# Kernel tuning notes

Measured on AMD Instinct MI355X. Metric: run time of the kernel, lower is better.

The kernel has to match this reference:

```python
import jax, jax.numpy as jnp
import numpy as np

B, C, H, W = 16, 384, 64, 64
S, R, GR = 16, 8, 64
EPS = 1e-6


def setup_inputs() -> dict:
    key = jax.random.key(0)
    ks = jax.random.split(key, 16)
    def rn(k, shape, s):
        return jax.random.normal(k, shape, dtype=jnp.float32) * s
    inp = {"x": jax.random.normal(ks[0], (B, C, H, W), dtype=jnp.float32)}
    i = 1
    for p in ("row", "col"):
        inp[p + "_a_logit"] = jnp.zeros((S,), jnp.float32)
        inp[p + "_U"] = rn(ks[i], (S, R), 0.02); i += 1
        inp[p + "_V"] = rn(ks[i], (S, R), 0.02); i += 1
        inp[p + "_Win"] = rn(ks[i], (S, C), 1.0 / np.sqrt(C)); i += 1
        inp[p + "_bin"] = jnp.zeros((S,), jnp.float32)
        inp[p + "_Wg"] = rn(ks[i], (S, C), 1.0 / np.sqrt(C)); i += 1
        inp[p + "_bg"] = jnp.zeros((S,), jnp.float32)
        inp[p + "_Wout"] = rn(ks[i], (C, S), 1.0 / np.sqrt(S)); i += 1
        inp[p + "_bout"] = jnp.zeros((C,), jnp.float32)
        inp[p + "_Wskip"] = rn(ks[i], (C, C), 1.0 / np.sqrt(C)); i += 1
        inp[p + "_bskip"] = jnp.zeros((C,), jnp.float32)
    inp["g1_w"] = rn(ks[i], (GR, C), 1.0 / np.sqrt(C)); i += 1
    inp["g1_b"] = jnp.zeros((GR,), jnp.float32)
    inp["g2_w"] = rn(ks[i], (C, GR), 1.0 / np.sqrt(GR)); i += 1
    inp["g2_b"] = jnp.zeros((C,), jnp.float32)
    inp["norm_w"] = jnp.ones((C,), jnp.float32)
    inp["norm_b"] = jnpp = jnp.zeros((C,), jnp.float32)
    inp["norm_b"] = jnp.zeros((C,), jnp.float32)
    return inp


def _ssm1d(x, a_logit, U, V, Win, bin_, Wg, bg, Wout, bout, Wskip, bskip, reverse):
    # x: [N, L, D]
    if reverse:
        x = x[:, ::-1]
    u = jnp.einsum('nld,sd->nls', x, Win) + bin_          # [N,L,S]
    g = jax.nn.sigmoid(jnp.einsum('nld,sd->nls', x, Wg) + bg)
    a = jax.nn.sigmoid(a_logit)                            # [S]
    # h_t = a*h + g_t*u_t + h @ (U V^T)^T  ==  h @ (diag(a) + (U V^T)^T) + g_t*u_t
    A = jnp.diag(a) + (U @ V.T).T                          # [S,S]
    gu = jnp.swapaxes(g * u, 0, 1)                         # [L,N,S]
    h0 = jnp.zeros((x.shape[0], a.shape[0]), x.dtype)

    def step(h, gu_t):
        h = h @ A + gu_t
        return h, h

    _, hs = jax.lax.scan(step, h0, gu)                     # [L,N,S]
    hs = jnp.swapaxes(hs, 0, 1)                            # [N,L,S]
    y = (jnp.einsum('nls,ds->nld', hs, Wout) + bout
         + jnp.einsum('nld,ed->nle', x, Wskip) + bskip)
    if reverse:
        y = y[:, ::-1]
    return y


def _forward(x, rp, cp, g1_w, g1_b, g2_w, g2_b, norm_w, norm_b):
    Bx, Cx, Hx, Wx = x.shape
    rows = jnp.transpose(x, (0, 2, 3, 1)).reshape(Bx * Hx, Wx, Cx)
    cols = jnp.transpose(x, (0, 3, 2, 1)).reshape(Bx * Wx, Hx, Cx)
    yr = _ssm1d(rows, *rp, False) + _ssm1d(rows, *rp, True)
    yc = _ssm1d(cols, *cp, False) + _ssm1d(cols, *cp, True)
    yr = jnp.transpose(yr.reshape(Bx, Hx, Wx, Cx), (0, 3, 1, 2))
    yc = jnp.transpose(yc.reshape(Bx, Wx, Hx, Cx), (0, 3, 2, 1))
    y = (yr + yc) * 0.25
    # LayerNorm over channel dim of BCHW
    mean = x.mean(axis=1, keepdims=True)
    var = ((x - mean) ** 2).mean(axis=1, keepdims=True)
    xn = (x - mean) / jnp.sqrt(var + EPS)
    xn = xn * norm_w[None, :, None, None] + norm_b[None, :, None, None]
    # gate: 1x1 conv -> GELU(exact) -> 1x1 conv -> sigmoid
    h1 = jax.nn.gelu(jnp.einsum('bchw,oc->bohw', xn, g1_w) + g1_b[None, :, None, None], approximate=False)
    g = jax.nn.sigmoid(jnp.einsum('bghw,cg->bchw', h1, g2_w) + g2_b[None, :, None, None])
    return g * y + (1.0 - g) * x


def reference(x, row_a_logit, row_U, row_V, row_Win, row_bin, row_Wg, row_bg, row_Wout, row_bout, row_Wskip, row_bskip, col_a_logit, col_U, col_V, col_Win, col_bin, col_Wg, col_bg, col_Wout, col_bout, col_Wskip, col_bskip, g1_w, g1_b, g2_w, g2_b, norm_w, norm_b):
    rp = (row_a_logit, row_U, row_V, row_Win, row_bin, row_Wg, row_bg, row_Wout, row_bout, row_Wskip, row_bskip)
    cp = (col_a_logit, col_U, col_V, col_Win, col_bin, col_Wg, col_bg, col_Wout, col_bout, col_Wskip, col_bskip)
    return _forward(x, rp, cp, g1_w, g1_b, g2_w, g2_b, norm_w, norm_b)
```

## Files before the change

kernel.cpp:

```cpp
#include <hip/hip_runtime.h>
#include <hip/hip_bf16.h>
#include <math.h>

#define PP 4096
#define CCH 384
#define NB 16

using short8 = __attribute__((ext_vector_type(8))) short;
using f32x4  = __attribute__((ext_vector_type(4))) float;

__device__ __forceinline__ float sigmoidf_(float v){ return 1.f/(1.f+expf(-v)); }
__device__ __forceinline__ unsigned int f2bf(float f){
  __hip_bfloat16 h = __float2bfloat16(f);
  return (unsigned int)*reinterpret_cast<unsigned short*>(&h);
}
__device__ __forceinline__ float bf2f(unsigned short u){
  unsigned int w = ((unsigned int)u) << 16;
  return __uint_as_float(w);
}
__device__ __forceinline__ void gload_lds16(const void* g, void* l){
  __builtin_amdgcn_global_load_lds(
      (const __attribute__((address_space(1))) unsigned int*)g,
      (__attribute__((address_space(3))) unsigned int*)l, 16, 0, 0);
}

__global__ __launch_bounds__(256) void k_prep(
    const float* __restrict__ rAl, const float* __restrict__ rU, const float* __restrict__ rV,
    const float* __restrict__ cAl, const float* __restrict__ cU, const float* __restrict__ cV,
    const float* __restrict__ rWs, const float* __restrict__ cWs,
    const float* __restrict__ WinR, const float* __restrict__ WgR,
    const float* __restrict__ WinC, const float* __restrict__ WgC,
    const float* __restrict__ g1w, const float* __restrict__ nw, const float* __restrict__ nb,
    const float* __restrict__ g2w,
    const float* __restrict__ WoR, const float* __restrict__ WoC,
    float* __restrict__ Arow, float* __restrict__ Acol,
    unsigned short* __restrict__ WsumBf, unsigned short* __restrict__ WcatBf,
    unsigned short* __restrict__ g2wBf, unsigned short* __restrict__ WocatBf,
    float* __restrict__ t1, float* __restrict__ t2)
{
  int bid = blockIdx.x, tid = threadIdx.x;
  if (bid < 576) {
    int idx = bid*256 + tid;
    WsumBf[idx] = (unsigned short)f2bf(rWs[idx] + cWs[idx]);
  } else if (bid < 768) {
    int idx = (bid-576)*256 + tid;
    int row = idx / CCH, col = idx - row*CCH;
    float v;
    if      (row < 16)  v = WinR[row*CCH + col];
    else if (row < 32)  v = WgR [(row-16)*CCH + col];
    else if (row < 48)  v = WinC[(row-32)*CCH + col];
    else if (row < 64)  v = WgC [(row-48)*CCH + col];
    else                v = g1w[(row-64)*CCH + col]*nw[col];
    WcatBf[idx] = (unsigned short)f2bf(v);
  } else if (bid < 864) {
    int idx = (bid-768)*256 + tid;
    g2wBf[idx] = (unsigned short)f2bf(g2w[idx]);
  } else if (bid < 912) {
    int idx = (bid-864)*256 + tid;
    int c = idx >> 5, k = idx & 31;
    float v = (k < 16) ? WoR[c*16 + k] : WoC[c*16 + (k-16)];
    WocatBf[idx] = (unsigned short)f2bf(v);
  } else {
    {
      int i = tid >> 4, j = tid & 15;
      float sr = 0.f, sc = 0.f;
      #pragma unroll
      for (int r=0;r<8;++r){ sr += rV[i*8+r]*rU[j*8+r]; sc += cV[i*8+r]*cU[j*8+r]; }
      if (i==j){ sr += sigmoidf_(rAl[i]); sc += sigmoidf_(cAl[i]); }
      Arow[tid] = sr; Acol[tid] = sc;
    }
    if (tid < 64) {
      float s1=0.f, s2=0.f;
      for (int c=0;c<CCH;++c){ s1 += g1w[tid*CCH+c]*nw[c]; s2 += nb[c]*g1w[tid*CCH+c]; }
      t1[tid]=s1; t2[tid]=s2;
    }
  }
}

__global__ __launch_bounds__(256) void k_xf(
    const float* __restrict__ x, const unsigned short* __restrict__ WcatBf,
    const float* __restrict__ binR, const float* __restrict__ bgR,
    const float* __restrict__ binC, const float* __restrict__ bgC,
    const float* __restrict__ t1, const float* __restrict__ t2,
    const float* __restrict__ g1b,
    unsigned short* __restrict__ xbf,
    float* __restrict__ ugr, float* __restrict__ ugc,
    unsigned short* __restrict__ h1bf)
{
  int b = blockIdx.x >> 6, pt = blockIdx.x & 63;
  int t = threadIdx.x;
  int w = t >> 6, l = t & 63;
  int lr = l & 15, kq = l >> 4, kb8 = kq*8;
  int pl = t & 63, g4 = w;

  __shared__ unsigned short xtb[64*64];
  __shared__ float red[512];
  __shared__ float meanS[64], invS[64];

  const float* xb = x + (size_t)b*CCH*PP + pt*64;
  f32x4 acc[2][4] = {};
  float sx = 0.f, sx2 = 0.f;

  float xv[16];
  #pragma unroll
  for (int j=0;j<16;++j) xv[j] = xb[(size_t)(g4*16 + j)*PP + pl];

  const unsigned short* wrow0 = WcatBf + (size_t)(w*32 + lr)*CCH + kb8;
  const unsigned short* wrow1 = wrow0 + 16*CCH;
  unsigned short* xgo = xbf + ((size_t)(b*PP + pt*64))*CCH;

  #pragma unroll
  for (int cc=0; cc<6; ++cc) {
    unsigned int pk[8];
    #pragma unroll
    for (int j=0;j<16;++j){ sx += xv[j]; sx2 += xv[j]*xv[j]; }
    #pragma unroll
    for (int j=0;j<8;++j) pk[j] = f2bf(xv[2*j]) | (f2bf(xv[2*j+1])<<16);
    __syncthreads();
    {
      int kg0 = g4*2, kg1 = g4*2+1;
      uint4 v0 = make_uint4(pk[0],pk[1],pk[2],pk[3]);
      uint4 v1 = make_uint4(pk[4],pk[5],pk[6],pk[7]);
      *(uint4*)&xtb[(size_t)(pl*8 + (kg0 ^ (pl&7)))*8] = v0;
      *(uint4*)&xtb[(size_t)(pl*8 + (kg1 ^ (pl&7)))*8] = v1;
    }
    if (cc < 5) {
      #pragma unroll
      for (int j=0;j<16;++j) xv[j] = xb[(size_t)((cc+1)*64 + g4*16 + j)*PP + pl];
    }
    short8 a0k0 = *(const short8*)(wrow0 + cc*64);
    short8 a0k1 = *(const short8*)(wrow0 + cc*64 + 32);
    short8 a1k0 = *(const short8*)(wrow1 + cc*64);
    short8 a1k1 = *(const short8*)(wrow1 + cc*64 + 32);
    __syncthreads();
    #pragma unroll
    for (int ks=0; ks<2; ++ks){
      int kg = ks*4 + kq;
      #pragma unroll
      for (int nf=0; nf<4; ++nf){
        int pr = nf*16 + lr;
        short8 bv = *(const short8*)&xtb[(size_t)(pr*8 + (kg ^ (pr&7)))*8];
        acc[0][nf] = __builtin_amdgcn_mfma_f32_16x16x32_bf16(ks? a0k1:a0k0, bv, acc[0][nf], 0,0,0);
        acc[1][nf] = __builtin_amdgcn_mfma_f32_16x16x32_bf16(ks? a1k1:a1k0, bv, acc[1][nf], 0,0,0);
      }
    }
    #pragma unroll
    for (int it=0; it<2; ++it){
      int p2 = 32*it + (t>>3), kg2 = t & 7;
      uint4 v = *(const uint4*)&xtb[(size_t)(p2*8 + (kg2 ^ (p2&7)))*8];
      *(uint4*)&xgo[(size_t)p2*CCH + cc*64 + kg2*8] = v;
    }
  }

  __syncthreads();
  red[g4*64 + pl] = sx;
  red[256 + g4*64 + pl] = sx2;
  __syncthreads();
  if (t < 64) {
    float s1 = red[t] + red[64+t] + red[128+t] + red[192+t];
    float s2 = red[256+t] + red[320+t] + red[384+t] + red[448+t];
    float mu = s1 * (1.f/CCH);
    float var = s2 * (1.f/CCH) - mu*mu;
    meanS[t] = mu;
    invS[t]  = rsqrtf(var + 1e-6f);
  }
  __syncthreads();

  if (w < 2) {
    const float* bu = w ? binC : binR;
    const float* bg = w ? bgC  : bgR;
    float* dst = w ? ugc : ugr;
    float bus[4], bgs[4];
    #pragma unroll
    for (int r=0;r<4;++r){ int s = kq*4 + r; bus[r]=bu[s]; bgs[r]=bg[s]; }
    #pragma unroll
    for (int nf=0; nf<4; ++nf){
      size_t pbase = ((size_t)(b*PP + pt*64 + nf*16 + lr))*16;
      #pragma unroll
      for (int r=0;r<4;++r){
        int s = kq*4 + r;
        float u = acc[0][nf][r] + bus[r];
        float g = sigmoidf_(acc[1][nf][r] + bgs[r]);
        dst[pbase + s] = u*g;
      }
    }
  } else {
    int ob = (w-2)*32 + kq*4;
    float t1o[2][4], t2o[2][4], gbo[2][4];
    #pragma unroll
    for (int mi=0;mi<2;++mi)
      #pragma unroll
      for (int r=0;r<4;++r){
        int o = ob + mi*16 + r;
        t1o[mi][r]=t1[o]; t2o[mi][r]=t2[o]; gbo[mi][r]=g1b[o];
      }
    #pragma unroll
    for (int nf=0; nf<4; ++nf){
      int pLoc = nf*16 + lr;
      float mu = meanS[pLoc], iv = invS[pLoc];
      #pragma unroll
      for (int mi=0;mi<2;++mi){
        unsigned int us[4];
        #pragma unroll
        for (int r=0;r<4;++r){
          float pre = iv*(acc[mi][nf][r] - mu*t1o[mi][r]) + t2o[mi][r] + gbo[mi][r];
          float ge = 0.5f*pre*(1.f + erff(pre*0.70710678118654752f));
          us[r] = f2bf(ge);
        }
        uint2 o2; o2.x = us[0] | (us[1]<<16); o2.y = us[2] | (us[3]<<16);
        *reinterpret_cast<uint2*>(h1bf + ((size_t)(b*PP + pt*64 + pLoc))*64 + (w-2)*32 + mi*16 + kq*4) = o2;
      }
    }
  }
}

__global__ __launch_bounds__(64) void k_scan(
    const float* __restrict__ ugr, const float* __restrict__ ugc,
    const float* __restrict__ Arow, const float* __restrict__ Acol,
    unsigned short* __restrict__ hscat)
{
  int g = blockIdx.x*4 + (threadIdx.x >> 4);
  int lane = threadIdx.x & 63;
  int s = lane & 15;
  int base = lane & 48;
  bool isCol = g >= 1024;
  int gg = isCol ? g - 1024 : g;
  int b = gg >> 6, rc = gg & 63;
  const float* ug = isCol ? ugc : ugr;
  const float* A  = isCol ? Acol : Arow;
  int off = isCol ? 16 : 0;
  int p0 = b*PP + (isCol ? rc : rc*64);
  int stride = isCol ? 64 : 1;
  float ac[16];
  #pragma unroll
  for (int i=0;i<16;++i) ac[i] = A[i*16 + s];
  float h[64];
  float hf = 0.f;
  #pragma unroll
  for (int l=0;l<64;++l){
    float gu = ug[((size_t)(p0 + l*stride))*16 + s];
    float t = 0.f;
    #pragma unroll
    for (int i=0;i<16;++i) t += __shfl(hf, base + i, 64) * ac[i];
    hf = t + gu;
    h[l] = hf;
  }
  float hb = 0.f;
  #pragma unroll
  for (int l=63;l>=0;--l){
    float gu = ug[((size_t)(p0 + l*stride))*16 + s];
    float t = 0.f;
    #pragma unroll
    for (int i=0;i<16;++i) t += __shfl(hb, base + i, 64) * ac[i];
    hb = t + gu;
    hscat[((size_t)(p0 + l*stride))*32 + off + s] = (unsigned short)f2bf(h[l] + hb);
  }
}

__global__ __launch_bounds__(512) void k_fused(
    const unsigned short* __restrict__ xbf,
    const unsigned short* __restrict__ WsumBf,
    const unsigned short* __restrict__ h1bf, const unsigned short* __restrict__ g2wBf,
    const unsigned short* __restrict__ hscat, const unsigned short* __restrict__ WocatBf,
    const float* __restrict__ g2b,
    const float* __restrict__ boR, const float* __restrict__ bsR,
    const float* __restrict__ boC, const float* __restrict__ bsC,
    float* __restrict__ outp)
{
  int obid = blockIdx.x;
  int bid = ((obid & 7) * 384) + (obid >> 3);
  int pt = bid & 63; int ct = (bid >> 6) % 3; int b = bid / 192;
  int t = threadIdx.x;
  int w = t >> 6, l = t & 63;
  int lr = l & 15, kq = l >> 4, kb8 = kq * 8;
  int c0 = ct*128;
  int crow = w*16 + kq*4;

  __shared__ unsigned short xt[64*48*8];

  short8 gaw[2], gbv[2][4];
  {
    const unsigned short* hbase = h1bf + ((size_t)(b*PP + pt*64 + lr))*64 + kb8;
    const unsigned short* wbg = g2wBf + (size_t)(c0 + w*16 + lr)*64 + kb8;
    #pragma unroll
    for (int ks=0; ks<2; ++ks){
      gaw[ks] = *(const short8*)(wbg + ks*32);
      #pragma unroll
      for (int nf=0; nf<4; ++nf)
        gbv[ks][nf] = *(const short8*)(hbase + (size_t)nf*16*64 + ks*32);
    }
  }

  {
    const unsigned short* xrow0 = xbf + ((size_t)(b*PP + pt*64))*CCH;
    #pragma unroll
    for (int i=0;i<6;++i){
      int G = w*384 + i*64 + l;
      int p = G/48, kgs = G - p*48;
      int kg = (kgs & ~7) | ((kgs & 7) ^ (p & 7));
      gload_lds16(xrow0 + (size_t)p*CCH + kg*8, &xt[(size_t)G*8]);
    }
  }

  f32x4 gac[4] = {};
  #pragma unroll
  for (int ks=0; ks<2; ++ks)
    #pragma unroll
    for (int nf=0; nf<4; ++nf)
      gac[nf] = __builtin_amdgcn_mfma_f32_16x16x32_bf16(gaw[ks], gbv[ks][nf], gac[nf], 0,0,0);

  __syncthreads();

  f32x4 accS[4] = {};
  const unsigned short* wbS = WsumBf + (size_t)(c0 + w*16 + lr)*CCH + kb8;
  #pragma unroll
  for (int c = 0; c < 6; ++c) {
    short8 a0 = *(const short8*)(wbS + c*64);
    short8 a1 = *(const short8*)(wbS + c*64 + 32);
    #pragma unroll
    for (int ks=0; ks<2; ++ks){
      int kgl = ks*4 + kq;
      #pragma unroll
      for (int nf=0; nf<4; ++nf){
        int pr = nf*16 + lr;
        int kgs = c*8 + (kgl ^ (pr & 7));
        short8 bv = *(const short8*)&xt[(size_t)(pr*48 + kgs)*8];
        accS[nf] = __builtin_amdgcn_mfma_f32_16x16x32_bf16(ks? a1:a0, bv, accS[nf], 0,0,0);
      }
    }
  }

  f32x4 yac[4] = {};
  {
    const unsigned short* hb2 = hscat + ((size_t)(b*PP + pt*64 + lr))*32 + kb8;
    const unsigned short* wo0 = WocatBf + (size_t)(c0 + w*16 + lr)*32 + kb8;
    short8 wa0 = *(const short8*)wo0;
    #pragma unroll
    for (int nf=0; nf<4; ++nf){
      short8 hv = *(const short8*)(hb2 + (size_t)nf*16*32);
      yac[nf] = __builtin_amdgcn_mfma_f32_16x16x32_bf16(wa0, hv, yac[nf], 0,0,0);
    }
  }

  uint2 xres[4];
  {
    int kR = c0 + crow;
    int kgR = kR >> 3, eoff = kR & 7;
    #pragma unroll
    for (int nf=0; nf<4; ++nf){
      int p = nf*16 + lr;
      int kgsR = (kgR & ~7) | ((kgR & 7) ^ (p & 7));
      xres[nf] = *(const uint2*)&xt[(size_t)(p*48 + kgsR)*8 + eoff];
    }
  }

  #pragma unroll
  for (int r=0;r<4;++r){
    int c = c0 + crow + r;
    float cbv = 2.f*(boR[c]+bsR[c]+boC[c]+bsC[c]);
    float gbv = g2b[c];
    #pragma unroll
    for (int nf=0;nf<4;++nf){
      unsigned int word = (r < 2) ? xres[nf].x : xres[nf].y;
      unsigned short us = (r & 1) ? (unsigned short)(word >> 16) : (unsigned short)(word & 0xffff);
      float xv = bf2f(us);
      size_t addr = ((size_t)(b*CCH + c))*PP + pt*64 + nf*16 + lr;
      float y = 0.25f*(yac[nf][r] + 2.f*accS[nf][r] + cbv);
      float gt = sigmoidf_(gac[nf][r] + gbv);
      outp[addr] = gt*y + (1.f-gt)*xv;
    }
  }
}

extern "C" void kernel_launch(void* const* d_in, const int* in_sizes, int n_in,
                              void* d_out, int out_size, void* d_ws, size_t ws_size,
                              hipStream_t stream)
{
  const float* x    = (const float*)d_in[0];
  const float* rAl  = (const float*)d_in[1];
  const float* rU   = (const float*)d_in[2];
  const float* rV   = (const float*)d_in[3];
  const float* rWin = (const float*)d_in[4];
  const float* rbin = (const float*)d_in[5];
  const float* rWg  = (const float*)d_in[6];
  const float* rbg  = (const float*)d_in[7];
  const float* rWo  = (const float*)d_in[8];
  const float* rbo  = (const float*)d_in[9];
  const float* rWs  = (const float*)d_in[10];
  const float* rbs  = (const float*)d_in[11];
  const float* cAl  = (const float*)d_in[12];
  const float* cU   = (const float*)d_in[13];
  const float* cV   = (const float*)d_in[14];
  const float* cWin = (const float*)d_in[15];
  const float* cbin = (const float*)d_in[16];
  const float* cWg  = (const float*)d_in[17];
  const float* cbg  = (const float*)d_in[18];
  const float* cWo  = (const float*)d_in[19];
  const float* cbo  = (const float*)d_in[20];
  const float* cWs  = (const float*)d_in[21];
  const float* cbs  = (const float*)d_in[22];
  const float* g1w  = (const float*)d_in[23];
  const float* g1b  = (const float*)d_in[24];
  const float* g2w  = (const float*)d_in[25];
  const float* g2b  = (const float*)d_in[26];
  const float* nw   = (const float*)d_in[27];
  const float* nb   = (const float*)d_in[28];

  float* ws   = (float*)d_ws;
  float* ugr  = ws;
  float* ugc  = ugr + 1048576;
  float* Arow = ugc + 1048576;
  float* Acol = Arow + 256;
  float* t1   = Acol + 256;
  float* t2   = t1 + 64;
  unsigned short* xbf     = (unsigned short*)(t2 + 64);
  unsigned short* h1bf    = xbf + (size_t)25165824;
  unsigned short* hscat   = h1bf + (size_t)4194304;
  unsigned short* WsumBf  = hscat + (size_t)2097152;
  unsigned short* WcatBf  = WsumBf + 147456;
  unsigned short* g2wBf   = WcatBf + 49152;
  unsigned short* WocatBf = g2wBf + 24576;
  float* outp = (float*)d_out;

  k_prep<<<913, 256, 0, stream>>>(rAl,rU,rV,cAl,cU,cV,rWs,cWs,
                                  rWin,rWg,cWin,cWg,g1w,nw,nb,g2w,rWo,cWo,
                                  Arow,Acol,WsumBf,WcatBf,g2wBf,WocatBf,t1,t2);
  k_xf<<<1024, 256, 0, stream>>>(x, WcatBf, rbin, rbg, cbin, cbg,
                                 t1, t2, g1b, xbf, ugr, ugc, h1bf);
  k_scan<<<512, 64, 0, stream>>>(ugr, ugc, Arow, Acol, hscat);
  k_fused<<<3072, 512, 0, stream>>>(xbf, WsumBf, h1bf, g2wBf,
                                    hscat, WocatBf, g2b,
                                    rbo, rbs, cbo, cbs, outp);
}
```

Before: 189.0 us.

## Split bidirectional scan into parallel directions and widen fused kernel channel tile

The scan kernel now runs forward and backward directions as separate parallel tasks, each writing its own slice of a wider hidden-state buffer. This removes the serial two-pass dependency and the 64-entry register array, at the cost of doubling hidden-state traffic. The fused output kernel now covers all 384 channels per pixel tile with 48 channels per wave, so the x tile in LDS and the h1/hs loads are reused across three channel groups instead of being reloaded by three separate blocks. The Wout folding absorbs the combine scaling, and sigmoid uses fast exp2/rcp intrinsics, with gate values packed to fp16 to limit register pressure.

```diff
diff --git a/kernel.cpp b/kernel.cpp
--- a/kernel.cpp
+++ b/kernel.cpp
@@ -8,8 +8,12 @@
 
 using short8 = __attribute__((ext_vector_type(8))) short;
 using f32x4  = __attribute__((ext_vector_type(4))) float;
+using half2t = __attribute__((ext_vector_type(2))) __fp16;
 
 __device__ __forceinline__ float sigmoidf_(float v){ return 1.f/(1.f+expf(-v)); }
+__device__ __forceinline__ float fast_sig(float v){
+  return __builtin_amdgcn_rcpf(1.f + __builtin_amdgcn_exp2f(-v*1.44269504088896f));
+}
 __device__ __forceinline__ unsigned int f2bf(float f){
   __hip_bfloat16 h = __float2bfloat16(f);
   return (unsigned int)*reinterpret_cast<unsigned short*>(&h);
@@ -55,10 +59,11 @@
   } else if (bid < 864) {
     int idx = (bid-768)*256 + tid;
     g2wBf[idx] = (unsigned short)f2bf(g2w[idx]);
-  } else if (bid < 912) {
+  } else if (bid < 960) {
     int idx = (bid-864)*256 + tid;
-    int c = idx >> 5, k = idx & 31;
-    float v = (k < 16) ? WoR[c*16 + k] : WoC[c*16 + (k-16)];
+    int c = idx >> 6, k = idx & 63;
+    int sel = (k >> 4) & 1;
+    float v = 0.5f * (sel ? WoC[c*16 + (k&15)] : WoR[c*16 + (k&15)]);
     WocatBf[idx] = (unsigned short)f2bf(v);
   } else {
     {
@@ -180,7 +185,7 @@
       for (int r=0;r<4;++r){
         int s = kq*4 + r;
         float u = acc[0][nf][r] + bus[r];
-        float g = sigmoidf_(acc[1][nf][r] + bgs[r]);
+        float g = fast_sig(acc[1][nf][r] + bgs[r]);
         dst[pbase + s] = u*g;
       }
     }
@@ -214,80 +219,74 @@
   }
 }
 
-__global__ __launch_bounds__(64) void k_scan(
+__global__ __launch_bounds__(256) void k_scan(
     const float* __restrict__ ugr, const float* __restrict__ ugc,
     const float* __restrict__ Arow, const float* __restrict__ Acol,
-    unsigned short* __restrict__ hscat)
+    unsigned short* __restrict__ hs2)
 {
-  int g = blockIdx.x*4 + (threadIdx.x >> 4);
+  int W = blockIdx.x*4 + (threadIdx.x >> 6);
   int lane = threadIdx.x & 63;
-  int s = lane & 15;
-  int base = lane & 48;
-  bool isCol = g >= 1024;
-  int gg = isCol ? g - 1024 : g;
+  int tsk = W*4 + (lane >> 4);
+  int s = lane & 15, base = lane & 48;
+  int dir = tsk >> 11;
+  int rem = tsk & 2047;
+  int isCol = rem >> 10;
+  int gg = rem & 1023;
   int b = gg >> 6, rc = gg & 63;
   const float* ug = isCol ? ugc : ugr;
   const float* A  = isCol ? Acol : Arow;
-  int off = isCol ? 16 : 0;
+  int off = dir*32 + isCol*16;
   int p0 = b*PP + (isCol ? rc : rc*64);
   int stride = isCol ? 64 : 1;
   float ac[16];
   #pragma unroll
   for (int i=0;i<16;++i) ac[i] = A[i*16 + s];
-  float h[64];
-  float hf = 0.f;
-  #pragma unroll
-  for (int l=0;l<64;++l){
-    float gu = ug[((size_t)(p0 + l*stride))*16 + s];
-    float t = 0.f;
-    #pragma unroll
-    for (int i=0;i<16;++i) t += __shfl(hf, base + i, 64) * ac[i];
-    hf = t + gu;
-    h[l] = hf;
-  }
-  float hb = 0.f;
-  #pragma unroll
-  for (int l=63;l>=0;--l){
-    float gu = ug[((size_t)(p0 + l*stride))*16 + s];
-    float t = 0.f;
-    #pragma unroll
-    for (int i=0;i<16;++i) t += __shfl(hb, base + i, 64) * ac[i];
-    hb = t + gu;
-    hscat[((size_t)(p0 + l*stride))*32 + off + s] = (unsigned short)f2bf(h[l] + hb);
-  }
-}
-
-__global__ __launch_bounds__(512) void k_fused(
+  float h = 0.f;
+  #pragma unroll 4
+  for (int st=0; st<64; ++st){
+    int l2 = dir ? (63-st) : st;
+    float gu = ug[((size_t)(p0 + l2*stride))*16 + s];
+    float tt = 0.f;
+    #pragma unroll
+    for (int i=0;i<16;++i) tt += __shfl(h, base + i, 64) * ac[i];
+    h = tt + gu;
+    hs2[((size_t)(p0 + l2*stride))*64 + off + s] = (unsigned short)f2bf(h);
+  }
+}
+
+__global__ __launch_bounds__(512, 4) void k_fused(
     const unsigned short* __restrict__ xbf,
     const unsigned short* __restrict__ WsumBf,
     const unsigned short* __restrict__ h1bf, const unsigned short* __restrict__ g2wBf,
-    const unsigned short* __restrict__ hscat, const unsigned short* __restrict__ WocatBf,
+    const unsigned short* __restrict__ hs2, const unsigned short* __restrict__ WocatBf,
     const float* __restrict__ g2b,
     const float* __restrict__ boR, const float* __restrict__ bsR,
     const float* __restrict__ boC, const float* __restrict__ bsC,
     float* __restrict__ outp)
 {
   int obid = blockIdx.x;
-  int bid = ((obid & 7) * 384) + (obid >> 3);
-  int pt = bid & 63; int ct = (bid >> 6) % 3; int b = bid / 192;
+  int bid = ((obid & 7) * 128) + (obid >> 3);
+  int b = bid >> 6, pt = bid & 63;
   int t = threadIdx.x;
   int w = t >> 6, l = t & 63;
   int lr = l & 15, kq = l >> 4, kb8 = kq * 8;
-  int c0 = ct*128;
-  int crow = w*16 + kq*4;
+  int cw = w*48;
 
   __shared__ unsigned short xt[64*48*8];
 
-  short8 gaw[2], gbv[2][4];
+  short8 gaw[3][2], gbv[2][4];
   {
     const unsigned short* hbase = h1bf + ((size_t)(b*PP + pt*64 + lr))*64 + kb8;
-    const unsigned short* wbg = g2wBf + (size_t)(c0 + w*16 + lr)*64 + kb8;
-    #pragma unroll
-    for (int ks=0; ks<2; ++ks){
-      gaw[ks] = *(const short8*)(wbg + ks*32);
+    #pragma unroll
+    for (int ks=0; ks<2; ++ks)
       #pragma unroll
       for (int nf=0; nf<4; ++nf)
         gbv[ks][nf] = *(const short8*)(hbase + (size_t)nf*16*64 + ks*32);
+    #pragma unroll
+    for (int mi=0; mi<3; ++mi){
+      const unsigned short* wbg = g2wBf + (size_t)(cw + mi*16 + lr)*64 + kb8;
+      gaw[mi][0] = *(const short8*)(wbg);
+      gaw[mi][1] = *(const short8*)(wbg + 32);
     }
   }
 
@@ -302,72 +301,110 @@
     }
   }
 
-  f32x4 gac[4] = {};
+  unsigned int gt[3][4][2];
+  {
+    f32x4 gac[3][4] = {};
+    #pragma unroll
+    for (int ks=0; ks<2; ++ks)
+      #pragma unroll
+      for (int nf=0; nf<4; ++nf)
+        #pragma unroll
+        for (int mi=0; mi<3; ++mi)
+          gac[mi][nf] = __builtin_amdgcn_mfma_f32_16x16x32_bf16(gaw[mi][ks], gbv[ks][nf], gac[mi][nf], 0,0,0);
+    #pragma unroll
+    for (int mi=0;mi<3;++mi){
+      float4 gb4 = *(const float4*)&g2b[cw + mi*16 + kq*4];
+      #pragma unroll
+      for (int nf=0;nf<4;++nf){
+        float s0 = fast_sig(gac[mi][nf][0] + gb4.x);
+        float s1 = fast_sig(gac[mi][nf][1] + gb4.y);
+        float s2 = fast_sig(gac[mi][nf][2] + gb4.z);
+        float s3 = fast_sig(gac[mi][nf][3] + gb4.w);
+        half2t p01 = __builtin_amdgcn_cvt_pkrtz(s0, s1);
+        half2t p23 = __builtin_amdgcn_cvt_pkrtz(s2, s3);
+        __builtin_memcpy(&gt[mi][nf][0], &p01, 4);
+        __builtin_memcpy(&gt[mi][nf][1], &p23, 4);
+      }
+    }
+  }
+
+  __syncthreads();
+
+  f32x4 acc[3][4] = {};
+  const unsigned short* wbS = WsumBf + (size_t)(cw + lr)*CCH + kb8;
   #pragma unroll
-  for (int ks=0; ks<2; ++ks)
-    #pragma unroll
-    for (int nf=0; nf<4; ++nf)
-      gac[nf] = __builtin_amdgcn_mfma_f32_16x16x32_bf16(gaw[ks], gbv[ks][nf], gac[nf], 0,0,0);
-
-  __syncthreads();
-
-  f32x4 accS[4] = {};
-  const unsigned short* wbS = WsumBf + (size_t)(c0 + w*16 + lr)*CCH + kb8;
-  #pragma unroll
-  for (int c = 0; c < 6; ++c) {
-    short8 a0 = *(const short8*)(wbS + c*64);
-    short8 a1 = *(const short8*)(wbS + c*64 + 32);
-    #pragma unroll
-    for (int ks=0; ks<2; ++ks){
+  for (int c=0;c<6;++c){
+    short8 a[3][2];
+    #pragma unroll
+    for (int mi=0;mi<3;++mi){
+      a[mi][0] = *(const short8*)(wbS + (size_t)mi*16*CCH + c*64);
+      a[mi][1] = *(const short8*)(wbS + (size_t)mi*16*CCH + c*64 + 32);
+    }
+    #pragma unroll
+    for (int ks=0;ks<2;++ks){
       int kgl = ks*4 + kq;
       #pragma unroll
-      for (int nf=0; nf<4; ++nf){
+      for (int nf=0;nf<4;++nf){
         int pr = nf*16 + lr;
         int kgs = c*8 + (kgl ^ (pr & 7));
         short8 bv = *(const short8*)&xt[(size_t)(pr*48 + kgs)*8];
-        accS[nf] = __builtin_amdgcn_mfma_f32_16x16x32_bf16(ks? a1:a0, bv, accS[nf], 0,0,0);
-      }
-    }
-  }
-
-  f32x4 yac[4] = {};
+        #pragma unroll
+        for (int mi=0;mi<3;++mi)
+          acc[mi][nf] = __builtin_amdgcn_mfma_f32_16x16x32_bf16(a[mi][ks], bv, acc[mi][nf], 0,0,0);
+      }
+    }
+  }
+
   {
-    const unsigned short* hb2 = hscat + ((size_t)(b*PP + pt*64 + lr))*32 + kb8;
-    const unsigned short* wo0 = WocatBf + (size_t)(c0 + w*16 + lr)*32 + kb8;
-    short8 wa0 = *(const short8*)wo0;
-    #pragma unroll
-    for (int nf=0; nf<4; ++nf){
-      short8 hv = *(const short8*)(hb2 + (size_t)nf*16*32);
-      yac[nf] = __builtin_amdgcn_mfma_f32_16x16x32_bf16(wa0, hv, yac[nf], 0,0,0);
-    }
-  }
-
-  uint2 xres[4];
-  {
-    int kR = c0 + crow;
-    int kgR = kR >> 3, eoff = kR & 7;
-    #pragma unroll
-    for (int nf=0; nf<4; ++nf){
+    const unsigned short* hb2 = hs2 + ((size_t)(b*PP + pt*64 + lr))*64 + kb8;
+    short8 hv[2][4];
+    #pragma unroll
+    for (int ks=0;ks<2;++ks)
+      #pragma unroll
+      for (int nf=0;nf<4;++nf)
+        hv[ks][nf] = *(const short8*)(hb2 + (size_t)nf*16*64 + ks*32);
+    #pragma unroll
+    for (int mi=0;mi<3;++mi){
+      const unsigned short* wo = WocatBf + (size_t)(cw + mi*16 + lr)*64 + kb8;
+      short8 wa0 = *(const short8*)(wo);
+      short8 wa1 = *(const short8*)(wo + 32);
+      #pragma unroll
+      for (int nf=0;nf<4;++nf){
+        acc[mi][nf] = __builtin_amdgcn_mfma_f32_16x16x32_bf16(wa0, hv[0][nf], acc[mi][nf], 0,0,0);
+        acc[mi][nf] = __builtin_amdgcn_mfma_f32_16x16x32_bf16(wa1, hv[1][nf], acc[mi][nf], 0,0,0);
+      }
+    }
+  }
+
+  #pragma unroll
+  for (int mi=0;mi<3;++mi){
+    int cb0 = cw + mi*16 + kq*4;
+    float4 b1 = *(const float4*)&boR[cb0];
+    float4 b2 = *(const float4*)&bsR[cb0];
+    float4 b3 = *(const float4*)&boC[cb0];
+    float4 b4 = *(const float4*)&bsC[cb0];
+    float cb4[4] = { b1.x+b2.x+b3.x+b4.x, b1.y+b2.y+b3.y+b4.y,
+                     b1.z+b2.z+b3.z+b4.z, b1.w+b2.w+b3.w+b4.w };
+    int kgR = cb0 >> 3, eoff = cb0 & 7;
+    #pragma unroll
+    for (int nf=0;nf<4;++nf){
       int p = nf*16 + lr;
       int kgsR = (kgR & ~7) | ((kgR & 7) ^ (p & 7));
-      xres[nf] = *(const uint2*)&xt[(size_t)(p*48 + kgsR)*8 + eoff];
-    }
-  }
-
-  #pragma unroll
-  for (int r=0;r<4;++r){
-    int c = c0 + crow + r;
-    float cbv = 2.f*(boR[c]+bsR[c]+boC[c]+bsC[c]);
-    float gbv = g2b[c];
-    #pragma unroll
-    for (int nf=0;nf<4;++nf){
-      unsigned int word = (r < 2) ? xres[nf].x : xres[nf].y;
-      unsigned short us = (r & 1) ? (unsigned short)(word >> 16) : (unsigned short)(word & 0xffff);
-      float xv = bf2f(us);
-      size_t addr = ((size_t)(b*CCH + c))*PP + pt*64 + nf*16 + lr;
-      float y = 0.25f*(yac[nf][r] + 2.f*accS[nf][r] + cbv);
-      float gt = sigmoidf_(gac[nf][r] + gbv);
-      outp[addr] = gt*y + (1.f-gt)*xv;
+      uint2 xres = *(const uint2*)&xt[(size_t)(p*48 + kgsR)*8 + eoff];
+      half2t g01, g23;
+      __builtin_memcpy(&g01, &gt[mi][nf][0], 4);
+      __builtin_memcpy(&g23, &gt[mi][nf][1], 4);
+      float gv[4] = { (float)g01[0], (float)g01[1], (float)g23[0], (float)g23[1] };
+      #pragma unroll
+      for (int r=0;r<4;++r){
+        unsigned int word = (r < 2) ? xres.x : xres.y;
+        unsigned short us = (r & 1) ? (unsigned short)(word >> 16) : (unsigned short)(word & 0xffff);
+        float xv = bf2f(us);
+        float y = 0.5f*acc[mi][nf][r] + 0.5f*cb4[r];
+        float gtv = gv[r];
+        size_t addr = ((size_t)(b*CCH + cb0 + r))*PP + pt*64 + p;
+        outp[addr] = gtv*y + (1.f-gtv)*xv;
+      }
     }
   }
 }
@@ -415,20 +452,20 @@
   float* t2   = t1 + 64;
   unsigned short* xbf     = (unsigned short*)(t2 + 64);
   unsigned short* h1bf    = xbf + (size_t)25165824;
-  unsigned short* hscat   = h1bf + (size_t)4194304;
-  unsigned short* WsumBf  = hscat + (size_t)2097152;
+  unsigned short* hs2     = h1bf + (size_t)4194304;
+  unsigned short* WsumBf  = hs2 + (size_t)4194304;
   unsigned short* WcatBf  = WsumBf + 147456;
   unsigned short* g2wBf   = WcatBf + 49152;
   unsigned short* WocatBf = g2wBf + 24576;
   float* outp = (float*)d_out;
 
-  k_prep<<<913, 256, 0, stream>>>(rAl,rU,rV,cAl,cU,cV,rWs,cWs,
+  k_prep<<<961, 256, 0, stream>>>(rAl,rU,rV,cAl,cU,cV,rWs,cWs,
                                   rWin,rWg,cWin,cWg,g1w,nw,nb,g2w,rWo,cWo,
                                   Arow,Acol,WsumBf,WcatBf,g2wBf,WocatBf,t1,t2);
   k_xf<<<1024, 256, 0, stream>>>(x, WcatBf, rbin, rbg, cbin, cbg,
                                  t1, t2, g1b, xbf, ugr, ugc, h1bf);
-  k_scan<<<512, 64, 0, stream>>>(ugr, ugc, Arow, Acol, hscat);
-  k_fused<<<3072, 512, 0, stream>>>(xbf, WsumBf, h1bf, g2wBf,
-                                    hscat, WocatBf, g2b,
+  k_scan<<<256, 256, 0, stream>>>(ugr, ugc, Arow, Acol, hs2);
+  k_fused<<<1024, 512, 0, stream>>>(xbf, WsumBf, h1bf, g2wBf,
+                                    hs2, WocatBf, g2b,
                                     rbo, rbs, cbo, cbs, outp);
 }
```

Measured after the change: 153.8 us (median of 3 runs). -18.6%, faster.
